# Performance work log

Hardware: AMD Instinct MI355X
Metric: run time of the kernel (lower is better)

Reference implementation:

```python
import jax, jax.numpy as jnp
import numpy as np

DIM = 1024
HEADS = 8


def setup_inputs() -> dict:
    key = jax.random.key(0)
    ks = jax.random.split(key, 8)
    b, n, m, nc, d = 2, 1024, 4, 1024, DIM
    x = jax.random.normal(ks[0], (b, n, d), dtype=jnp.float32)
    context = jax.random.normal(ks[1], (b, m, nc, d), dtype=jnp.float32)
    doc_similarities = jax.random.normal(ks[2], (b, m), dtype=jnp.float32)
    # learned params (Linear weights stored as [in, out] for x @ W)
    s = 1.0 / np.sqrt(d)
    Wq = jax.random.uniform(ks[3], (d, d), minval=-s, maxval=s, dtype=jnp.float32)
    Wkv = jax.random.uniform(ks[4], (d, 2 * d), minval=-s, maxval=s, dtype=jnp.float32)
    Wout = jax.random.uniform(ks[5], (d, d), minval=-s, maxval=s, dtype=jnp.float32)
    bout = jax.random.uniform(ks[6], (d,), minval=-s, maxval=s, dtype=jnp.float32)
    beta = jnp.array(1.0, dtype=jnp.float32)
    return {"x": x, "context": context, "doc_similarities": doc_similarities,
            "Wq": Wq, "Wkv": Wkv, "beta": beta, "Wout": Wout, "bout": bout}


def reference(x, context, doc_similarities, Wq, Wkv, beta, Wout, bout):
    b, n, dim = x.shape
    h = HEADS
    hd = dim // h
    scale = dim ** -0.5
    m, nc = context.shape[1], context.shape[2]

    # q: [b, h, n, hd]
    q = (x @ Wq).reshape(b, n, h, hd).transpose(0, 2, 1, 3)

    # flatten docs: [b, m*nc, dim]
    ctx = context.reshape(b, m * nc, dim)
    # doc similarity bias, repeated per token within each doc: [b, m*nc]
    sim = jnp.repeat(doc_similarities, nc, axis=1) * beta

    kv = ctx @ Wkv  # [b, L, 2*dim]
    k, v = jnp.split(kv, 2, axis=-1)
    k = k.reshape(b, m * nc, h, hd).transpose(0, 2, 1, 3)  # [b, h, L, hd]
    v = v.reshape(b, m * nc, h, hd).transpose(0, 2, 1, 3)

    dots = jnp.einsum('bhid,bhjd->bhij', q, k) * scale
    dots = dots + sim[:, None, None, :]
    attn = jax.nn.softmax(dots, axis=-1)
    out = jnp.einsum('bhij,bhjd->bhid', attn, v)
    out = out.transpose(0, 2, 1, 3).reshape(b, n, dim)
    return out @ Wout + bout
```

## Files before the change

kernel.cpp:

```cpp
#include <hip/hip_runtime.h>
#include <stdint.h>

typedef __attribute__((ext_vector_type(4))) float f32x4;
typedef __attribute__((ext_vector_type(8))) __bf16 bf16x8;

__device__ __forceinline__ uint16_t f2bf(float f) {
  uint32_t u = __builtin_bit_cast(uint32_t, f);
  u += 0x7FFFu + ((u >> 16) & 1u);
  return (uint16_t)(u >> 16);
}

__device__ __forceinline__ float bf2f(uint16_t u) {
  uint32_t v = ((uint32_t)u) << 16;
  return __builtin_bit_cast(float, v);
}

__device__ __forceinline__ void load_lds16(const uint16_t* g, uint16_t* l) {
  __builtin_amdgcn_global_load_lds((const __attribute__((address_space(1))) void*)g,
                                   (__attribute__((address_space(3))) void*)l, 16, 0, 0);
}

__global__ __launch_bounds__(256) void k_prep(const float* __restrict__ x,
                                              const float* __restrict__ ctx,
                                              const float* __restrict__ Wq,
                                              const float* __restrict__ Wkv,
                                              const float* __restrict__ Wout,
                                              uint16_t* __restrict__ xb,
                                              uint16_t* __restrict__ ctxb,
                                              uint16_t* __restrict__ wqt,
                                              uint16_t* __restrict__ wkvt,
                                              uint16_t* __restrict__ woutt,
                                              float qscale) {
  __shared__ float tile[32][33];
  int id = blockIdx.x;
  int tid = threadIdx.x;
  if (id < 10240) {
    const float* in;
    uint16_t* out;
    int j = id * 256 + tid;
    if (j < 524288) { in = x; out = xb; }
    else            { in = ctx; out = ctxb; j -= 524288; }
    float4 v = ((const float4*)in)[j];
    union { uint16_t u[4]; uint64_t q; } o;
    o.u[0] = f2bf(v.x); o.u[1] = f2bf(v.y); o.u[2] = f2bf(v.z); o.u[3] = f2bf(v.w);
    ((uint64_t*)out)[j] = o.q;
    return;
  }
  id -= 10240;
  const float* W;
  uint16_t* Wt;
  int N, n0, k0;
  float sc = 1.0f;
  if (id < 1024)      { W = Wq;   Wt = wqt;   N = 1024; sc = qscale;
                        n0 = (id & 31) * 32; k0 = (id >> 5) * 32; }
  else if (id < 2048) { W = Wout; Wt = woutt; N = 1024; id -= 1024;
                        n0 = (id & 31) * 32; k0 = (id >> 5) * 32; }
  else                { W = Wkv;  Wt = wkvt;  N = 2048; id -= 2048;
                        n0 = (id & 63) * 32; k0 = (id >> 6) * 32; }
  int c = tid & 31, r0 = tid >> 5;
#pragma unroll
  for (int i = 0; i < 4; i++) {
    int r = r0 + i * 8;
    tile[r][c] = W[(size_t)(k0 + r) * N + n0 + c];
  }
  __syncthreads();
#pragma unroll
  for (int i = 0; i < 4; i++) {
    int r = r0 + i * 8;
    Wt[(size_t)(n0 + r) * 1024 + k0 + c] = f2bf(tile[c][r] * sc);
  }
}

__global__ __launch_bounds__(256, 4) void k_gemm_fused(const uint16_t* __restrict__ ctxb,
                                                       const uint16_t* __restrict__ wkvt,
                                                       const uint16_t* __restrict__ xb,
                                                       const uint16_t* __restrict__ wqt,
                                                       uint16_t* __restrict__ kb,
                                                       uint16_t* __restrict__ vtb,
                                                       uint16_t* __restrict__ qb) {
  __shared__ uint16_t smem[16384];
  const int K = 1024;
  const int tid = threadIdx.x;
  const int lane = tid & 63, w = tid >> 6;
  const int quad = lane >> 4, l16 = lane & 15;
  const int wr = (w >> 1) * 64, wc = (w & 1) * 64;
  int id = blockIdx.x;
  int bx, by, isQ;
  const uint16_t *Ab, *Bb;
  if (id < 1024) {
    isQ = 0;
    int xcd = id & 7, t = id >> 3;
    by = (xcd << 3) + (t & 7);
    bx = t >> 3;
    Ab = ctxb + (size_t)by * 128 * K;
    Bb = wkvt + (size_t)bx * 128 * K;
  } else {
    isQ = 1; id -= 1024;
    int xcd = id & 7, t = id >> 3;
    by = (xcd << 1) + (t & 1);
    bx = t >> 1;
    Ab = xb + (size_t)by * 128 * K;
    Bb = wqt + (size_t)bx * 128 * K;
  }
  f32x4 acc[4][4] = {};
  const int rA = tid >> 2, slotA = tid & 3;
  const int rA1 = rA + 64;
  const int segA0 = (slotA ^ ((rA + (rA >> 2)) & 3)) * 8;
  const int segA1 = (slotA ^ ((rA1 + (rA1 >> 2)) & 3)) * 8;
  const uint16_t* gA0 = Ab + (size_t)rA * K + segA0;
  const uint16_t* gA1 = Ab + (size_t)rA1 * K + segA1;
  const uint16_t* gB0 = Bb + (size_t)rA * K + segA0;
  const uint16_t* gB1 = Bb + (size_t)rA1 * K + segA1;
  load_lds16(gA0, smem + tid * 8);
  load_lds16(gA1, smem + (tid + 256) * 8);
  load_lds16(gB0, smem + (tid + 512) * 8);
  load_lds16(gB1, smem + (tid + 768) * 8);
  for (int t = 0; t < 32; ++t) {
    const uint16_t* la = smem + (t & 1) * 8192;
    const uint16_t* lb = la + 4096;
    if (t < 31) {
      uint16_t* ln = smem + ((t + 1) & 1) * 8192;
      const int k1 = (t + 1) * 32;
      load_lds16(gA0 + k1, ln + tid * 8);
      load_lds16(gA1 + k1, ln + (tid + 256) * 8);
      load_lds16(gB0 + k1, ln + (tid + 512) * 8);
      load_lds16(gB1 + k1, ln + (tid + 768) * 8);
      asm volatile("s_waitcnt vmcnt(4)\n\ts_barrier" ::: "memory");
    } else {
      asm volatile("s_waitcnt vmcnt(0)\n\ts_barrier" ::: "memory");
    }
    bf16x8 af[4], bfr[4];
#pragma unroll
    for (int i = 0; i < 4; i++) {
      int R = wr + i * 16 + l16;
      int s = quad ^ ((R + (R >> 2)) & 3);
      af[i] = *(const bf16x8*)&la[R * 32 + s * 8];
    }
#pragma unroll
    for (int j = 0; j < 4; j++) {
      int R = wc + j * 16 + l16;
      int s = quad ^ ((R + (R >> 2)) & 3);
      bfr[j] = *(const bf16x8*)&lb[R * 32 + s * 8];
    }
    __builtin_amdgcn_s_setprio(1);
#pragma unroll
    for (int i = 0; i < 4; i++)
#pragma unroll
      for (int j = 0; j < 4; j++)
        acc[i][j] = __builtin_amdgcn_mfma_f32_16x16x32_bf16(af[i], bfr[j], acc[i][j], 0, 0, 0);
    __builtin_amdgcn_s_setprio(0);
    asm volatile("s_barrier" ::: "memory");
  }
  __syncthreads();
  if (isQ) {
#pragma unroll
    for (int i = 0; i < 4; i++)
#pragma unroll
      for (int j = 0; j < 4; j++) {
        size_t row = (size_t)by * 128 + wr + i * 16 + quad * 4;
        size_t col = (size_t)bx * 128 + wc + j * 16 + l16;
#pragma unroll
        for (int r = 0; r < 4; r++)
          qb[(row + r) * 1024 + col] = f2bf(acc[i][j][r]);
      }
  } else if (bx < 8) {
#pragma unroll
    for (int i = 0; i < 4; i++)
#pragma unroll
      for (int j = 0; j < 4; j++) {
        int rowg = by * 128 + wr + i * 16 + quad * 4;
        int bb = rowg >> 12, l = rowg & 4095;
        int c = wc + j * 16 + l16;
        uint16_t* dst = kb + (((size_t)(bb * 8 + bx) * 4096 + l) * 128 + c);
#pragma unroll
        for (int r = 0; r < 4; r++)
          dst[r * 128] = f2bf(acc[i][j][r]);
      }
  } else {
    const int bh = (by >> 5) * 8 + (bx - 8);
    const int lbase = (by & 31) * 128;
    uint16_t* vdst = vtb + (size_t)bh * 524288;
#pragma unroll
    for (int half = 0; half < 2; half++) {
      if (wr == half * 64) {
#pragma unroll
        for (int i = 0; i < 4; i++)
#pragma unroll
          for (int j = 0; j < 4; j++) {
            int rowl = i * 16 + quad * 4;
            int col = wc + j * 16 + l16;
            union { uint64_t q; uint16_t u[4]; } pk;
#pragma unroll
            for (int r = 0; r < 4; r++) pk.u[r] = f2bf(acc[i][j][r]);
            *(uint64_t*)&smem[col * 72 + rowl] = pk.q;
          }
      }
      __syncthreads();
      {
        int col = tid >> 1, rseg = (tid & 1) * 32;
        const uint16_t* src = &smem[col * 72 + rseg];
        uint16_t* d = vdst + (size_t)col * 4096 + lbase + half * 64 + rseg;
#pragma unroll
        for (int k = 0; k < 4; k++)
          ((uint4*)d)[k] = *(const uint4*)&src[k * 8];
      }
      __syncthreads();
    }
  }
}

__global__ __launch_bounds__(256) void k_gemm64(const uint16_t* __restrict__ A,
                                                const uint16_t* __restrict__ Bt,
                                                float* __restrict__ Cf,
                                                const float* __restrict__ bias,
                                                int M, int N, int K) {
  __shared__ uint16_t smem[16384];
  const int tid = threadIdx.x;
  const int lane = tid & 63, w = tid >> 6;
  const int quad = lane >> 4, l16 = lane & 15;
  const int wr = (w >> 1) * 32, wc = (w & 1) * 32;
  const size_t tr0 = (size_t)blockIdx.y * 64, tc0 = (size_t)blockIdx.x * 64;
  f32x4 acc[2][2] = {};
  const int rS = tid >> 3, sS = tid & 7;
  const int seg = (sS ^ (rS & 7)) * 8;
  const uint16_t* Ab = A + tr0 * K;
  const uint16_t* Bb = Bt + tc0 * K;
  const uint16_t* gA0 = Ab + (size_t)rS * K + seg;
  const uint16_t* gA1 = Ab + (size_t)(rS + 32) * K + seg;
  const uint16_t* gB0 = Bb + (size_t)rS * K + seg;
  const uint16_t* gB1 = Bb + (size_t)(rS + 32) * K + seg;
  const int NT = K >> 6;
  load_lds16(gA0, smem + tid * 8);
  load_lds16(gA1, smem + (tid + 256) * 8);
  load_lds16(gB0, smem + (tid + 512) * 8);
  load_lds16(gB1, smem + (tid + 768) * 8);
  for (int t = 0; t < NT; ++t) {
    const uint16_t* la = smem + (t & 1) * 8192;
    const uint16_t* lb = la + 4096;
    if (t < NT - 1) {
      uint16_t* ln = smem + ((t + 1) & 1) * 8192;
      const int k1 = (t + 1) * 64;
      load_lds16(gA0 + k1, ln + tid * 8);
      load_lds16(gA1 + k1, ln + (tid + 256) * 8);
      load_lds16(gB0 + k1, ln + (tid + 512) * 8);
      load_lds16(gB1 + k1, ln + (tid + 768) * 8);
      asm volatile("s_waitcnt vmcnt(4)\n\ts_barrier" ::: "memory");
    } else {
      asm volatile("s_waitcnt vmcnt(0)\n\ts_barrier" ::: "memory");
    }
    __builtin_amdgcn_s_setprio(1);
#pragma unroll
    for (int sub = 0; sub < 2; sub++) {
      const int kk = sub * 4 + quad;
      bf16x8 af[2], bfr[2];
#pragma unroll
      for (int i = 0; i < 2; i++) {
        int R = wr + i * 16 + l16;
        af[i] = *(const bf16x8*)&la[R * 64 + (kk ^ (R & 7)) * 8];
      }
#pragma unroll
      for (int j = 0; j < 2; j++) {
        int R = wc + j * 16 + l16;
        bfr[j] = *(const bf16x8*)&lb[R * 64 + (kk ^ (R & 7)) * 8];
      }
#pragma unroll
      for (int i = 0; i < 2; i++)
#pragma unroll
        for (int j = 0; j < 2; j++)
          acc[i][j] = __builtin_amdgcn_mfma_f32_16x16x32_bf16(af[i], bfr[j], acc[i][j], 0, 0, 0);
    }
    __builtin_amdgcn_s_setprio(0);
    asm volatile("s_barrier" ::: "memory");
  }
#pragma unroll
  for (int i = 0; i < 2; i++) {
#pragma unroll
    for (int j = 0; j < 2; j++) {
      size_t row = tr0 + wr + i * 16 + quad * 4;
      size_t col = tc0 + wc + j * 16 + l16;
#pragma unroll
      for (int r = 0; r < 4; r++)
        Cf[(row + r) * N + col] = acc[i][j][r] + bias[col];
    }
  }
}

__global__ __launch_bounds__(256) void k_attn(const uint16_t* __restrict__ q,
                                              const uint16_t* __restrict__ kb,
                                              const uint16_t* __restrict__ vt,
                                              const float* __restrict__ sims,
                                              const float* __restrict__ beta,
                                              uint16_t* __restrict__ po,
                                              float* __restrict__ pl) {
  __shared__ uint16_t Kl[8192];
  __shared__ uint16_t Vl[8192];
  __shared__ uint16_t Pl[4096];
  const int idx = blockIdx.x;
  const int qbx = idx >> 7, g = idx & 127;
  const int h = g >> 4, b = (g >> 3) & 1, sp = g & 7;
  const int q0 = qbx * 128;
  const int tid = threadIdx.x, lane = tid & 63, w = tid >> 6;
  const int quad = lane >> 4, l16 = lane & 15;
  const float wsplit =
      __builtin_amdgcn_exp2f(sims[b * 4 + (sp >> 1)] * beta[0] * 1.44269504f);
  uint16_t* Pw = Pl + w * 1024;

  union { uint32_t u[4]; bf16x8 v; } Oc;
#pragma unroll
  for (int j = 0; j < 4; j++) Oc.u[j] = 0x3F803F80u;
  const bf16x8 onesf = Oc.v;

  bf16x8 qf[2][4];
#pragma unroll
  for (int rb = 0; rb < 2; rb++) {
    const uint16_t* qrow =
        q + ((size_t)(b * 1024 + q0 + w * 32 + rb * 16 + l16)) * 1024 + h * 128 + quad * 8;
#pragma unroll
    for (int ks = 0; ks < 4; ks++) qf[rb][ks] = *(const bf16x8*)(qrow + ks * 32);
  }
  f32x4 o[2][8] = {};
  f32x4 o9[2] = {};

  const uint16_t* kptr = kb + ((size_t)(b * 8 + h) * 4096 + sp * 512) * 128;
  const uint16_t* vptr = vt + ((size_t)(b * 8 + h) * 128) * 4096 + sp * 512;

  for (int c = 0; c < 8; c++) {
    __syncthreads();
#pragma unroll
    for (int ii = 0; ii < 4; ii++) {
      int g2 = tid + ii * 256;
      int row = g2 >> 4, seg = (g2 & 15) ^ (row & 15);
      load_lds16(kptr + row * 128 + seg * 8, Kl + g2 * 8);
    }
#pragma unroll
    for (int ii = 0; ii < 4; ii++) {
      int g2 = tid + ii * 256;
      int row = g2 >> 3, seg = (g2 & 7) ^ (row & 7);
      load_lds16(vptr + (size_t)row * 4096 + seg * 8, Vl + g2 * 8);
    }
    __syncthreads();
#pragma unroll
    for (int kh = 0; kh < 2; kh++) {
#pragma unroll
      for (int nb2 = 0; nb2 < 2; nb2++) {
        const int nb = kh * 2 + nb2;
        f32x4 s0 = {}, s1 = {};
#pragma unroll
        for (int ks = 0; ks < 4; ks++) {
          bf16x8 kf = *(const bf16x8*)&Kl[(nb * 16 + l16) * 128 + (((ks * 4 + quad) ^ l16) * 8)];
          s0 = __builtin_amdgcn_mfma_f32_16x16x32_bf16(qf[0][ks], kf, s0, 0, 0, 0);
          s1 = __builtin_amdgcn_mfma_f32_16x16x32_bf16(qf[1][ks], kf, s1, 0, 0, 0);
        }
        const int sl = nb2 * 2 + (l16 >> 3);
#pragma unroll
        for (int r = 0; r < 4; r++) {
          int rp0 = quad * 4 + r;
          Pw[rp0 * 32 + ((sl ^ ((rp0 >> 1) & 3)) * 8) + (l16 & 7)] =
              f2bf(__builtin_amdgcn_exp2f(s0[r]));
          int rp1 = 16 + rp0;
          Pw[rp1 * 32 + ((sl ^ ((rp1 >> 1) & 3)) * 8) + (l16 & 7)] =
              f2bf(__builtin_amdgcn_exp2f(s1[r]));
        }
      }
      __asm__ volatile("s_waitcnt lgkmcnt(0)" ::: "memory");
      const int segp = (quad ^ ((l16 >> 1) & 3)) * 8;
      bf16x8 pf0 = *(const bf16x8*)&Pw[l16 * 32 + segp];
      bf16x8 pf1 = *(const bf16x8*)&Pw[(16 + l16) * 32 + segp];
      const int sq = ((kh * 4 + quad) ^ (l16 & 7)) * 8;
#pragma unroll
      for (int nb = 0; nb < 8; nb++) {
        bf16x8 vf = *(const bf16x8*)&Vl[(nb * 16 + l16) * 64 + sq];
        o[0][nb] = __builtin_amdgcn_mfma_f32_16x16x32_bf16(pf0, vf, o[0][nb], 0, 0, 0);
        o[1][nb] = __builtin_amdgcn_mfma_f32_16x16x32_bf16(pf1, vf, o[1][nb], 0, 0, 0);
      }
      o9[0] = __builtin_amdgcn_mfma_f32_16x16x32_bf16(pf0, onesf, o9[0], 0, 0, 0);
      o9[1] = __builtin_amdgcn_mfma_f32_16x16x32_bf16(pf1, onesf, o9[1], 0, 0, 0);
    }
    kptr += 64 * 128;
    vptr += 64;
  }
  const int rowbase = (sp * 16 + b * 8 + h) * 1024 + q0 + w * 32;
#pragma unroll
  for (int rb = 0; rb < 2; rb++)
#pragma unroll
    for (int r = 0; r < 4; r++) {
      int row = rowbase + rb * 16 + quad * 4 + r;
#pragma unroll
      for (int nb = 0; nb < 8; nb++)
        po[(size_t)row * 128 + nb * 16 + l16] = f2bf(o[rb][nb][r] * wsplit);
      if (l16 == 0)
        pl[row] = o9[rb][r] * wsplit;
    }
}

__global__ __launch_bounds__(256) void k_merge(const uint16_t* __restrict__ po,
                                               const float* __restrict__ pl,
                                               uint16_t* __restrict__ attb) {
  const int bq = blockIdx.x;
  const int b = bq >> 10, qi = bq & 1023;
  const int t = threadIdx.x;
  const int h = t >> 5, d0 = (t & 31) * 4;
  const int bh = b * 8 + h;
  float den = 0.f;
  float acc[4] = {0.f, 0.f, 0.f, 0.f};
#pragma unroll
  for (int s = 0; s < 8; s++) {
    den += pl[(s * 16 + bh) * 1024 + qi];
    union { uint64_t q; uint16_t u[4]; } v;
    v.q = *(const uint64_t*)&po[(((size_t)(s * 16 + bh)) * 1024 + qi) * 128 + d0];
#pragma unroll
    for (int j = 0; j < 4; j++) acc[j] += bf2f(v.u[j]);
  }
  const float inv = 1.0f / den;
  union { uint64_t q; uint16_t u[4]; } o;
#pragma unroll
  for (int j = 0; j < 4; j++) o.u[j] = f2bf(acc[j] * inv);
  *(uint64_t*)&attb[((size_t)(b * 1024 + qi)) * 1024 + h * 128 + d0] = o.q;
}

extern "C" void kernel_launch(void* const* d_in, const int* in_sizes, int n_in,
                              void* d_out, int out_size, void* d_ws, size_t ws_size,
                              hipStream_t stream) {
  (void)in_sizes; (void)n_in; (void)out_size; (void)ws_size;
  const float* x    = (const float*)d_in[0];
  const float* ctx  = (const float*)d_in[1];
  const float* sims = (const float*)d_in[2];
  const float* Wq   = (const float*)d_in[3];
  const float* Wkv  = (const float*)d_in[4];
  const float* beta = (const float*)d_in[5];
  const float* Wout = (const float*)d_in[6];
  const float* bout = (const float*)d_in[7];
  float* out = (float*)d_out;

  char* ws = (char*)d_ws;
  uint16_t* xb    = (uint16_t*)(ws + 0);
  uint16_t* ctxb  = (uint16_t*)(ws + (4u << 20));
  uint16_t* wqt   = (uint16_t*)(ws + (20u << 20));
  uint16_t* wkvt  = (uint16_t*)(ws + (22u << 20));
  uint16_t* kb    = (uint16_t*)(ws + (32u << 20));
  uint16_t* vtb   = (uint16_t*)(ws + (48u << 20));
  float*    pl    = (float*)   (ws + (64u << 20));
  uint16_t* woutt = (uint16_t*)(ws + (68u << 20));
  uint16_t* qb    = (uint16_t*)(ws + (70u << 20));
  uint16_t* attb  = (uint16_t*)(ws + (74u << 20));
  uint16_t* po = (uint16_t*)(ws + 0);

  const float LOG2E = 1.44269504f;
  const float qscale = 0.03125f * LOG2E;

  k_prep<<<14336, 256, 0, stream>>>(x, ctx, Wq, Wkv, Wout, xb, ctxb, wqt, wkvt, woutt, qscale);
  k_gemm_fused<<<1152, 256, 0, stream>>>(ctxb, wkvt, xb, wqt, kb, vtb, qb);
  k_attn<<<1024, 256, 0, stream>>>(qb, kb, vtb, sims, beta, po, pl);
  k_merge<<<2048, 256, 0, stream>>>(po, pl, attb);
  k_gemm64<<<dim3(16, 32), 256, 0, stream>>>(attb, woutt, out, bout, 2048, 1024, 1024);
}
```

Before: 221.8 us.

## Double-buffer K/V tiles in attention kernel and raise MFMA wave priority

The attention kernel now keeps two LDS buffers for K and V and issues the async global-to-LDS loads for the next chunk before computing on the current one. It waits with a partial vmcnt so the current chunk's loads are complete while the next chunk's stay in flight, and adds a barrier at the end of each iteration to protect buffer reuse. MFMA sections are wrapped in s_setprio to favour matrix work. This is meant to hide global load latency behind compute, at the cost of doubling LDS use (about 72KB), which may reduce occupancy.

```diff
diff --git a/kernel.cpp b/kernel.cpp
--- a/kernel.cpp
+++ b/kernel.cpp
@@ -292,8 +292,8 @@
                                               const float* __restrict__ beta,
                                               uint16_t* __restrict__ po,
                                               float* __restrict__ pl) {
-  __shared__ uint16_t Kl[8192];
-  __shared__ uint16_t Vl[8192];
+  __shared__ uint16_t Kl[2][8192];
+  __shared__ uint16_t Vl[2][8192];
   __shared__ uint16_t Pl[4096];
   const int idx = blockIdx.x;
   const int qbx = idx >> 7, g = idx & 127;
@@ -324,33 +324,57 @@
   const uint16_t* kptr = kb + ((size_t)(b * 8 + h) * 4096 + sp * 512) * 128;
   const uint16_t* vptr = vt + ((size_t)(b * 8 + h) * 128) * 4096 + sp * 512;
 
+#pragma unroll
+  for (int ii = 0; ii < 4; ii++) {
+    int g2 = tid + ii * 256;
+    int row = g2 >> 4, seg = (g2 & 15) ^ (row & 15);
+    load_lds16(kptr + row * 128 + seg * 8, &Kl[0][g2 * 8]);
+  }
+#pragma unroll
+  for (int ii = 0; ii < 4; ii++) {
+    int g2 = tid + ii * 256;
+    int row = g2 >> 3, seg = (g2 & 7) ^ (row & 7);
+    load_lds16(vptr + (size_t)row * 4096 + seg * 8, &Vl[0][g2 * 8]);
+  }
+
   for (int c = 0; c < 8; c++) {
-    __syncthreads();
-#pragma unroll
-    for (int ii = 0; ii < 4; ii++) {
-      int g2 = tid + ii * 256;
-      int row = g2 >> 4, seg = (g2 & 15) ^ (row & 15);
-      load_lds16(kptr + row * 128 + seg * 8, Kl + g2 * 8);
-    }
-#pragma unroll
-    for (int ii = 0; ii < 4; ii++) {
-      int g2 = tid + ii * 256;
-      int row = g2 >> 3, seg = (g2 & 7) ^ (row & 7);
-      load_lds16(vptr + (size_t)row * 4096 + seg * 8, Vl + g2 * 8);
-    }
-    __syncthreads();
+    const uint16_t* Kc = Kl[c & 1];
+    const uint16_t* Vc = Vl[c & 1];
+    if (c < 7) {
+      const uint16_t* kn = kptr + 64 * 128;
+      const uint16_t* vn = vptr + 64;
+      uint16_t* Kd = Kl[(c + 1) & 1];
+      uint16_t* Vd = Vl[(c + 1) & 1];
+#pragma unroll
+      for (int ii = 0; ii < 4; ii++) {
+        int g2 = tid + ii * 256;
+        int row = g2 >> 4, seg = (g2 & 15) ^ (row & 15);
+        load_lds16(kn + row * 128 + seg * 8, Kd + g2 * 8);
+      }
+#pragma unroll
+      for (int ii = 0; ii < 4; ii++) {
+        int g2 = tid + ii * 256;
+        int row = g2 >> 3, seg = (g2 & 7) ^ (row & 7);
+        load_lds16(vn + (size_t)row * 4096 + seg * 8, Vd + g2 * 8);
+      }
+      asm volatile("s_waitcnt vmcnt(8)\n\ts_barrier" ::: "memory");
+    } else {
+      asm volatile("s_waitcnt vmcnt(0)\n\ts_barrier" ::: "memory");
+    }
 #pragma unroll
     for (int kh = 0; kh < 2; kh++) {
 #pragma unroll
       for (int nb2 = 0; nb2 < 2; nb2++) {
         const int nb = kh * 2 + nb2;
         f32x4 s0 = {}, s1 = {};
+        __builtin_amdgcn_s_setprio(1);
 #pragma unroll
         for (int ks = 0; ks < 4; ks++) {
-          bf16x8 kf = *(const bf16x8*)&Kl[(nb * 16 + l16) * 128 + (((ks * 4 + quad) ^ l16) * 8)];
+          bf16x8 kf = *(const bf16x8*)&Kc[(nb * 16 + l16) * 128 + (((ks * 4 + quad) ^ l16) * 8)];
           s0 = __builtin_amdgcn_mfma_f32_16x16x32_bf16(qf[0][ks], kf, s0, 0, 0, 0);
           s1 = __builtin_amdgcn_mfma_f32_16x16x32_bf16(qf[1][ks], kf, s1, 0, 0, 0);
         }
+        __builtin_amdgcn_s_setprio(0);
         const int sl = nb2 * 2 + (l16 >> 3);
 #pragma unroll
         for (int r = 0; r < 4; r++) {
@@ -367,15 +391,18 @@
       bf16x8 pf0 = *(const bf16x8*)&Pw[l16 * 32 + segp];
       bf16x8 pf1 = *(const bf16x8*)&Pw[(16 + l16) * 32 + segp];
       const int sq = ((kh * 4 + quad) ^ (l16 & 7)) * 8;
+      __builtin_amdgcn_s_setprio(1);
 #pragma unroll
       for (int nb = 0; nb < 8; nb++) {
-        bf16x8 vf = *(const bf16x8*)&Vl[(nb * 16 + l16) * 64 + sq];
+        bf16x8 vf = *(const bf16x8*)&Vc[(nb * 16 + l16) * 64 + sq];
         o[0][nb] = __builtin_amdgcn_mfma_f32_16x16x32_bf16(pf0, vf, o[0][nb], 0, 0, 0);
         o[1][nb] = __builtin_amdgcn_mfma_f32_16x16x32_bf16(pf1, vf, o[1][nb], 0, 0, 0);
       }
       o9[0] = __builtin_amdgcn_mfma_f32_16x16x32_bf16(pf0, onesf, o9[0], 0, 0, 0);
       o9[1] = __builtin_amdgcn_mfma_f32_16x16x32_bf16(pf1, onesf, o9[1], 0, 0, 0);
-    }
+      __builtin_amdgcn_s_setprio(0);
+    }
+    asm volatile("s_barrier" ::: "memory");
     kptr += 64 * 128;
     vptr += 64;
   }
```

Result: no change. 221.7 us (-0.1%).
